# Kernel optimization log

Hardware: AMD Instinct MI355X
Metric: run time of the kernel (lower is better)

Reference implementation:

```python
import jax, jax.numpy as jnp
import numpy as np

N, C, L, NUM_LAYERS = 512, 32, 1024, 3
BN_EPS = 1e-5


def setup_inputs() -> dict:
    key = jax.random.key(0)
    kx, kw, kb, kg, kbe = jax.random.split(key, 5)
    x = jax.random.normal(kx, (N, C, L), dtype=jnp.float32)
    # Per-channel, per-layer Linear weights: (C, num_layers, L_out, L_in)
    W = jax.random.normal(kw, (C, NUM_LAYERS, L, L), dtype=jnp.float32) / np.float32(np.sqrt(L))
    b = 0.01 * jax.random.normal(kb, (C, NUM_LAYERS, L), dtype=jnp.float32)
    # BatchNorm affine params for the num_layers-1 inner BN layers
    gamma = 1.0 + 0.1 * jax.random.normal(kg, (C, NUM_LAYERS - 1, L), dtype=jnp.float32)
    beta = 0.1 * jax.random.normal(kbe, (C, NUM_LAYERS - 1, L), dtype=jnp.float32)
    return {"x": x, "W": W, "b": b, "gamma": gamma, "beta": beta}


def reference(x, W, b, gamma, beta):
    """Fused per-channel MLP head.

    x: (N, C, L). For each channel c, applies num_layers Linear layers with
    ReLU + BatchNorm1d (training-mode batch stats, biased variance) between
    layers. All C channels computed as one batched GEMM per layer.
    """
    h = x
    for i in range(NUM_LAYERS):
        # batched per-channel Linear: (N,C,Lin) x (C,Lout,Lin) -> (N,C,Lout)
        h = jnp.einsum('ncl,cml->ncm', h, W[:, i]) + b[:, i][None]
        if i < NUM_LAYERS - 1:
            h = jax.nn.relu(h)
            # BatchNorm1d over the batch dim N, per (channel, feature)
            mean = jnp.mean(h, axis=0)          # (C, L)
            var = jnp.var(h, axis=0)            # biased variance, matches torch BN
            h = (h - mean) * jax.lax.rsqrt(var + BN_EPS) * gamma[:, i] + beta[:, i]
    return h
```

## Files before the change

kernel.cpp:

```cpp
#include <hip/hip_runtime.h>
#include <hip/hip_bf16.h>

#define NB 512
#define CCH 32
#define LF 1024
#define CL (CCH * LF)
#define BN_EPS 1e-5f

typedef __bf16 bf16x8 __attribute__((ext_vector_type(8)));
typedef __bf16 bf16x4 __attribute__((ext_vector_type(4)));
typedef float f32x4 __attribute__((ext_vector_type(4)));

#define QSTRIDE 1032

template <bool BNA, bool RELU>
__global__ __launch_bounds__(256, 2) void gemm_k(
    const float* __restrict__ Abase, const float* __restrict__ Wall,
    const float* __restrict__ ball, const float* __restrict__ scale,
    const float* __restrict__ shift, float* __restrict__ Out, int layer) {
  __shared__ __bf16 As[4 * QSTRIDE];
  __shared__ __bf16 Bs[4 * QSTRIDE];

  const int tid = threadIdx.x;
  const int c = blockIdx.y;
  const int mtile = blockIdx.x & 3;
  const int ntile = blockIdx.x >> 2;

  const float* A = Abase + c * LF;
  const float* Wp = Wall + (size_t)(c * 3 + layer) * LF * LF;
  const float* bias = ball + (c * 3 + layer) * LF;
  const float* scl = BNA ? scale + c * LF : nullptr;
  const float* shf = BNA ? shift + c * LF : nullptr;

  const int lane = tid & 63;
  const int wv = tid >> 6;
  const int wm = (wv & 1) * 64;
  const int wn = (wv >> 1) * 64;
  const int l15 = lane & 15;
  const int quad = lane >> 4;

  const int sr = tid >> 3;
  const int kseg = tid & 7;
  const int q = kseg >> 1;
  const int bsub = (kseg & 1) * 4;

  f32x4 acc[4][4] = {};

  for (int kt = 0; kt < LF / 32; ++kt) {
    const int k0 = kt * 32 + kseg * 4;

    f32x4 sc, sh;
    if (BNA) {
      sc = *(const f32x4*)(scl + k0);
      sh = *(const f32x4*)(shf + k0);
    }
#pragma unroll
    for (int i = 0; i < 4; ++i) {
      const int r = i * 32 + sr;
      f32x4 v = *(const f32x4*)(A + (size_t)(mtile * 128 + r) * CL + k0);
      if (BNA) v = v * sc + sh;
      bf16x4 o = {(__bf16)v.x, (__bf16)v.y, (__bf16)v.z, (__bf16)v.w};
      *(bf16x4*)&As[q * QSTRIDE + r * 8 + bsub] = o;
    }
#pragma unroll
    for (int i = 0; i < 4; ++i) {
      const int r = i * 32 + sr;
      f32x4 v = *(const f32x4*)(Wp + (size_t)(ntile * 128 + r) * LF + k0);
      bf16x4 o = {(__bf16)v.x, (__bf16)v.y, (__bf16)v.z, (__bf16)v.w};
      *(bf16x4*)&Bs[q * QSTRIDE + r * 8 + bsub] = o;
    }
    __syncthreads();

    bf16x8 af[4], bfr[4];
#pragma unroll
    for (int mi = 0; mi < 4; ++mi)
      af[mi] = *(const bf16x8*)&As[quad * QSTRIDE + (wm + mi * 16 + l15) * 8];
#pragma unroll
    for (int ni = 0; ni < 4; ++ni)
      bfr[ni] = *(const bf16x8*)&Bs[quad * QSTRIDE + (wn + ni * 16 + l15) * 8];
#pragma unroll
    for (int mi = 0; mi < 4; ++mi)
#pragma unroll
      for (int ni = 0; ni < 4; ++ni)
        acc[mi][ni] = __builtin_amdgcn_mfma_f32_16x16x32_bf16(
            af[mi], bfr[ni], acc[mi][ni], 0, 0, 0);
    __syncthreads();
  }

  float* outp = Out + (size_t)c * LF;
#pragma unroll
  for (int ni = 0; ni < 4; ++ni) {
    const int feat = ntile * 128 + wn + ni * 16 + l15;
    const float bv = bias[feat];
#pragma unroll
    for (int mi = 0; mi < 4; ++mi) {
      const int row0 = mtile * 128 + wm + mi * 16 + quad * 4;
#pragma unroll
      for (int r = 0; r < 4; ++r) {
        float v = acc[mi][ni][r] + bv;
        if (RELU) v = fmaxf(v, 0.f);
        outp[(size_t)(row0 + r) * CL + feat] = v;
      }
    }
  }
}

__global__ __launch_bounds__(256) void bn_stats(
    const float* __restrict__ H, const float* __restrict__ gamma,
    const float* __restrict__ beta, float* __restrict__ scale,
    float* __restrict__ shift, int bnlayer) {
  __shared__ float s_sum[256], s_sq[256];
  const int tid = threadIdx.x;
  const int f = tid & 63, g = tid >> 6;
  const int c = blockIdx.y;
  const int l = blockIdx.x * 64 + f;
  const float* col = H + (size_t)c * LF + l;
  float sum = 0.f, sq = 0.f;
  for (int n = g; n < NB; n += 4) {
    float v = col[(size_t)n * CL];
    sum += v;
    sq += v * v;
  }
  s_sum[tid] = sum;
  s_sq[tid] = sq;
  __syncthreads();
  if (g == 0) {
    sum = s_sum[f] + s_sum[64 + f] + s_sum[128 + f] + s_sum[192 + f];
    sq = s_sq[f] + s_sq[64 + f] + s_sq[128 + f] + s_sq[192 + f];
    const float mean = sum * (1.f / NB);
    const float var = sq * (1.f / NB) - mean * mean;
    const float rstd = rsqrtf(var + BN_EPS);
    const float ga = gamma[(size_t)(c * 2 + bnlayer) * LF + l];
    const float be = beta[(size_t)(c * 2 + bnlayer) * LF + l];
    const float sc = rstd * ga;
    scale[(size_t)c * LF + l] = sc;
    shift[(size_t)c * LF + l] = be - mean * sc;
  }
}

extern "C" void kernel_launch(void* const* d_in, const int* in_sizes, int n_in,
                              void* d_out, int out_size, void* d_ws,
                              size_t ws_size, hipStream_t stream) {
  const float* x = (const float*)d_in[0];
  const float* W = (const float*)d_in[1];
  const float* b = (const float*)d_in[2];
  const float* gamma = (const float*)d_in[3];
  const float* beta = (const float*)d_in[4];
  float* out = (float*)d_out;

  float* scale0 = (float*)d_ws;
  float* shift0 = scale0 + CCH * LF;
  float* scale1 = shift0 + CCH * LF;
  float* shift1 = scale1 + CCH * LF;
  float* h2 = shift1 + CCH * LF;

  const dim3 blk(256);
  const dim3 ggrid(32, 32);
  const dim3 sgrid(16, 32);

  gemm_k<false, true><<<ggrid, blk, 0, stream>>>(x, W, b, nullptr, nullptr, out, 0);
  bn_stats<<<sgrid, blk, 0, stream>>>(out, gamma, beta, scale0, shift0, 0);
  gemm_k<true, true><<<ggrid, blk, 0, stream>>>(out, W, b, scale0, shift0, h2, 1);
  bn_stats<<<sgrid, blk, 0, stream>>>(h2, gamma, beta, scale1, shift1, 1);
  gemm_k<true, false><<<ggrid, blk, 0, stream>>>(h2, W, b, scale1, shift1, out, 2);
}
```

Baseline: 941.7 us.

## Double-buffer GEMM tiles, store intermediates as bf16 channel-major, remap block grid

Adds register-staged double buffering to the GEMM K-loop, so global loads for the next K-slice are issued before the MFMAs on the current slice and a single barrier per iteration remains. Intermediate activations h1/h2 are now stored as bf16 in a channel-major [C][N][L] layout, which halves their traffic and makes the next layer's A reads contiguous. The LDS layout changes to row-major with padding, and the 1D grid groups 8 channels per tile index, presumably to improve cache locality. Rounding the intermediates to bf16 adds slight precision loss before the BN statistics are computed.

```diff
diff --git a/kernel.cpp b/kernel.cpp
--- a/kernel.cpp
+++ b/kernel.cpp
@@ -6,107 +6,162 @@
 #define LF 1024
 #define CL (CCH * LF)
 #define BN_EPS 1e-5f
+#define LSE 40
 
 typedef __bf16 bf16x8 __attribute__((ext_vector_type(8)));
 typedef __bf16 bf16x4 __attribute__((ext_vector_type(4)));
 typedef float f32x4 __attribute__((ext_vector_type(4)));
 
-#define QSTRIDE 1032
-
-template <bool BNA, bool RELU>
+template <bool AF32, bool BNA, bool RELU, bool OUTBF>
 __global__ __launch_bounds__(256, 2) void gemm_k(
-    const float* __restrict__ Abase, const float* __restrict__ Wall,
+    const void* __restrict__ Ain, const float* __restrict__ W,
     const float* __restrict__ ball, const float* __restrict__ scale,
-    const float* __restrict__ shift, float* __restrict__ Out, int layer) {
-  __shared__ __bf16 As[4 * QSTRIDE];
-  __shared__ __bf16 Bs[4 * QSTRIDE];
+    const float* __restrict__ shift, void* __restrict__ Out, int layer) {
+  __shared__ __bf16 As[2 * 128 * LSE];
+  __shared__ __bf16 Bs[2 * 128 * LSE];
 
   const int tid = threadIdx.x;
-  const int c = blockIdx.y;
-  const int mtile = blockIdx.x & 3;
-  const int ntile = blockIdx.x >> 2;
-
-  const float* A = Abase + c * LF;
-  const float* Wp = Wall + (size_t)(c * 3 + layer) * LF * LF;
-  const float* bias = ball + (c * 3 + layer) * LF;
-  const float* scl = BNA ? scale + c * LF : nullptr;
-  const float* shf = BNA ? shift + c * LF : nullptr;
-
-  const int lane = tid & 63;
-  const int wv = tid >> 6;
-  const int wm = (wv & 1) * 64;
-  const int wn = (wv >> 1) * 64;
-  const int l15 = lane & 15;
-  const int quad = lane >> 4;
-
-  const int sr = tid >> 3;
-  const int kseg = tid & 7;
-  const int q = kseg >> 1;
-  const int bsub = (kseg & 1) * 4;
+  const int bid = blockIdx.x;
+  const int c = (bid & 7) | ((bid >> 8) << 3);
+  const int tile = (bid >> 3) & 31;
+  const int mtile = tile & 3;
+  const int ntile = tile >> 2;
+
+  const int lane = tid & 63, wv = tid >> 6;
+  const int wm = (wv & 1) * 64, wn = (wv >> 1) * 64;
+  const int l15 = lane & 15, quad = lane >> 4;
+
+  const int sr = tid >> 3, kseg = tid & 7;
+  const float* Wp =
+      W + ((size_t)(c * 3 + layer) * LF + ntile * 128 + wv * 32) * LF;
+
+  const float* Axf = (const float*)Ain + (size_t)c * LF;
+  const __bf16* Axb = (const __bf16*)Ain + (size_t)c * NB * LF;
+  const float* scl = BNA ? scale + (size_t)c * LF + kseg * 4 : nullptr;
+  const float* shf = BNA ? shift + (size_t)c * LF + kseg * 4 : nullptr;
 
   f32x4 acc[4][4] = {};
-
-  for (int kt = 0; kt < LF / 32; ++kt) {
-    const int k0 = kt * 32 + kseg * 4;
-
-    f32x4 sc, sh;
-    if (BNA) {
-      sc = *(const f32x4*)(scl + k0);
-      sh = *(const f32x4*)(shf + k0);
-    }
-#pragma unroll
-    for (int i = 0; i < 4; ++i) {
-      const int r = i * 32 + sr;
-      f32x4 v = *(const f32x4*)(A + (size_t)(mtile * 128 + r) * CL + k0);
-      if (BNA) v = v * sc + sh;
-      bf16x4 o = {(__bf16)v.x, (__bf16)v.y, (__bf16)v.z, (__bf16)v.w};
-      *(bf16x4*)&As[q * QSTRIDE + r * 8 + bsub] = o;
-    }
-#pragma unroll
-    for (int i = 0; i < 4; ++i) {
-      const int r = i * 32 + sr;
-      f32x4 v = *(const f32x4*)(Wp + (size_t)(ntile * 128 + r) * LF + k0);
-      bf16x4 o = {(__bf16)v.x, (__bf16)v.y, (__bf16)v.z, (__bf16)v.w};
-      *(bf16x4*)&Bs[q * QSTRIDE + r * 8 + bsub] = o;
-    }
-    __syncthreads();
-
+  f32x4 va[4], vb[4], sc, sh;
+
+#define LOADA(k0)                                                           \
+  {                                                                         \
+    _Pragma("unroll") for (int i = 0; i < 4; ++i) {                         \
+      const int r = mtile * 128 + i * 32 + sr;                              \
+      if (AF32) {                                                           \
+        va[i] = *(const f32x4*)(Axf + (size_t)r * CL + (k0) + kseg * 4);    \
+      } else {                                                              \
+        bf16x4 t = *(const bf16x4*)(Axb + (size_t)r * LF + (k0) + kseg * 4);\
+        va[i] = f32x4{(float)t[0], (float)t[1], (float)t[2], (float)t[3]};  \
+      }                                                                     \
+    }                                                                       \
+    if (BNA) {                                                              \
+      sc = *(const f32x4*)(scl + (k0));                                     \
+      sh = *(const f32x4*)(shf + (k0));                                     \
+    }                                                                       \
+  }
+#define LOADB(k0)                                                           \
+  {                                                                         \
+    _Pragma("unroll") for (int j = 0; j < 4; ++j) {                         \
+      const int fl = j * 64 + lane;                                         \
+      vb[j] =                                                               \
+          *(const f32x4*)(Wp + (size_t)(fl >> 3) * LF + (k0) + (fl & 7) * 4);\
+    }                                                                       \
+  }
+#define WRITEAB(dstA, dstB)                                                 \
+  {                                                                         \
+    _Pragma("unroll") for (int i = 0; i < 4; ++i) {                         \
+      f32x4 v = va[i];                                                      \
+      if (BNA) v = v * sc + sh;                                             \
+      bf16x4 o = {(__bf16)v[0], (__bf16)v[1], (__bf16)v[2], (__bf16)v[3]};  \
+      *(bf16x4*)&(dstA)[(i * 32 + sr) * LSE + kseg * 4] = o;                \
+    }                                                                       \
+    _Pragma("unroll") for (int j = 0; j < 4; ++j) {                         \
+      const int fl = j * 64 + lane;                                         \
+      f32x4 w = vb[j];                                                      \
+      bf16x4 o = {(__bf16)w[0], (__bf16)w[1], (__bf16)w[2], (__bf16)w[3]};  \
+      *(bf16x4*)&(dstB)[(wv * 32 + (fl >> 3)) * LSE + (fl & 7) * 4] = o;    \
+    }                                                                       \
+  }
+
+  LOADA(0);
+  LOADB(0);
+  WRITEAB(As, Bs);
+  __syncthreads();
+
+  int buf = 0;
+  for (int kt = 0; kt < 32; ++kt) {
+    if (kt < 31) {
+      const int k0n = (kt + 1) * 32;
+      LOADA(k0n);
+      LOADB(k0n);
+    }
+    const __bf16* Ac = As + buf * (128 * LSE);
+    const __bf16* Bc = Bs + buf * (128 * LSE);
     bf16x8 af[4], bfr[4];
 #pragma unroll
     for (int mi = 0; mi < 4; ++mi)
-      af[mi] = *(const bf16x8*)&As[quad * QSTRIDE + (wm + mi * 16 + l15) * 8];
+      af[mi] = *(const bf16x8*)&Ac[(wm + mi * 16 + l15) * LSE + quad * 8];
 #pragma unroll
     for (int ni = 0; ni < 4; ++ni)
-      bfr[ni] = *(const bf16x8*)&Bs[quad * QSTRIDE + (wn + ni * 16 + l15) * 8];
+      bfr[ni] = *(const bf16x8*)&Bc[(wn + ni * 16 + l15) * LSE + quad * 8];
 #pragma unroll
     for (int mi = 0; mi < 4; ++mi)
 #pragma unroll
       for (int ni = 0; ni < 4; ++ni)
         acc[mi][ni] = __builtin_amdgcn_mfma_f32_16x16x32_bf16(
             af[mi], bfr[ni], acc[mi][ni], 0, 0, 0);
+    if (kt < 31) {
+      __bf16* An = As + (buf ^ 1) * (128 * LSE);
+      __bf16* Bn = Bs + (buf ^ 1) * (128 * LSE);
+      WRITEAB(An, Bn);
+    }
     __syncthreads();
-  }
-
-  float* outp = Out + (size_t)c * LF;
-#pragma unroll
-  for (int ni = 0; ni < 4; ++ni) {
-    const int feat = ntile * 128 + wn + ni * 16 + l15;
-    const float bv = bias[feat];
-#pragma unroll
-    for (int mi = 0; mi < 4; ++mi) {
-      const int row0 = mtile * 128 + wm + mi * 16 + quad * 4;
-#pragma unroll
-      for (int r = 0; r < 4; ++r) {
-        float v = acc[mi][ni][r] + bv;
-        if (RELU) v = fmaxf(v, 0.f);
-        outp[(size_t)(row0 + r) * CL + feat] = v;
+    buf ^= 1;
+  }
+
+  const float* bias = ball + (size_t)(c * 3 + layer) * LF;
+  if (OUTBF) {
+    __bf16* outp = (__bf16*)Out + (size_t)c * NB * LF;
+#pragma unroll
+    for (int ni = 0; ni < 4; ++ni) {
+      const int feat = ntile * 128 + wn + ni * 16 + l15;
+      const float bvv = bias[feat];
+#pragma unroll
+      for (int mi = 0; mi < 4; ++mi) {
+        const int row0 = mtile * 128 + wm + mi * 16 + quad * 4;
+#pragma unroll
+        for (int r = 0; r < 4; ++r) {
+          float vv = acc[mi][ni][r] + bvv;
+          if (RELU) vv = fmaxf(vv, 0.f);
+          outp[(size_t)(row0 + r) * LF + feat] = (__bf16)vv;
+        }
       }
     }
-  }
+  } else {
+    float* outp = (float*)Out + (size_t)c * LF;
+#pragma unroll
+    for (int ni = 0; ni < 4; ++ni) {
+      const int feat = ntile * 128 + wn + ni * 16 + l15;
+      const float bvv = bias[feat];
+#pragma unroll
+      for (int mi = 0; mi < 4; ++mi) {
+        const int row0 = mtile * 128 + wm + mi * 16 + quad * 4;
+#pragma unroll
+        for (int r = 0; r < 4; ++r) {
+          float vv = acc[mi][ni][r] + bvv;
+          if (RELU) vv = fmaxf(vv, 0.f);
+          outp[(size_t)(row0 + r) * CL + feat] = vv;
+        }
+      }
+    }
+  }
+#undef LOADA
+#undef LOADB
+#undef WRITEAB
 }
 
 __global__ __launch_bounds__(256) void bn_stats(
-    const float* __restrict__ H, const float* __restrict__ gamma,
+    const __bf16* __restrict__ H, const float* __restrict__ gamma,
     const float* __restrict__ beta, float* __restrict__ scale,
     float* __restrict__ shift, int bnlayer) {
   __shared__ float s_sum[256], s_sq[256];
@@ -114,10 +169,10 @@
   const int f = tid & 63, g = tid >> 6;
   const int c = blockIdx.y;
   const int l = blockIdx.x * 64 + f;
-  const float* col = H + (size_t)c * LF + l;
+  const __bf16* col = H + (size_t)c * NB * LF + l;
   float sum = 0.f, sq = 0.f;
   for (int n = g; n < NB; n += 4) {
-    float v = col[(size_t)n * CL];
+    float v = (float)col[(size_t)n * LF];
     sum += v;
     sq += v * v;
   }
@@ -148,19 +203,22 @@
   const float* beta = (const float*)d_in[4];
   float* out = (float*)d_out;
 
-  float* scale0 = (float*)d_ws;
-  float* shift0 = scale0 + CCH * LF;
-  float* scale1 = shift0 + CCH * LF;
-  float* shift1 = scale1 + CCH * LF;
-  float* h2 = shift1 + CCH * LF;
+  char* ws = (char*)d_ws;
+  float* scale = (float*)ws;  ws += (size_t)CL * 4;
+  float* shift = (float*)ws;  ws += (size_t)CL * 4;
+  __bf16* h1 = (__bf16*)ws;   ws += (size_t)NB * CL * 2;
+  __bf16* h2 = (__bf16*)ws;
 
   const dim3 blk(256);
-  const dim3 ggrid(32, 32);
+  const int ggrid = 1024;
   const dim3 sgrid(16, 32);
 
-  gemm_k<false, true><<<ggrid, blk, 0, stream>>>(x, W, b, nullptr, nullptr, out, 0);
-  bn_stats<<<sgrid, blk, 0, stream>>>(out, gamma, beta, scale0, shift0, 0);
-  gemm_k<true, true><<<ggrid, blk, 0, stream>>>(out, W, b, scale0, shift0, h2, 1);
-  bn_stats<<<sgrid, blk, 0, stream>>>(h2, gamma, beta, scale1, shift1, 1);
-  gemm_k<true, false><<<ggrid, blk, 0, stream>>>(h2, W, b, scale1, shift1, out, 2);
+  gemm_k<true, false, true, true>
+      <<<ggrid, blk, 0, stream>>>(x, W, b, nullptr, nullptr, h1, 0);
+  bn_stats<<<sgrid, blk, 0, stream>>>(h1, gamma, beta, scale, shift, 0);
+  gemm_k<false, true, true, true>
+      <<<ggrid, blk, 0, stream>>>(h1, W, b, scale, shift, h2, 1);
+  bn_stats<<<sgrid, blk, 0, stream>>>(h2, gamma, beta, scale, shift, 1);
+  gemm_k<false, true, false, false>
+      <<<ggrid, blk, 0, stream>>>(h2, W, b, scale, shift, out, 2);
 }
```

Result: faster. 825.9 us (-12.3%).
